# Performance work log

Hardware: AMD Instinct MI355X
Metric: run time of the kernel (lower is better)

Reference implementation:

```python
import jax, jax.numpy as jnp
import numpy as np

D_MODEL = 512
NHEAD = 8
WINDOW = 32  # attends to [i-32, i+32]


def setup_inputs() -> dict:
    key = jax.random.key(0)
    ks = jax.random.split(key, 5)
    B, S, D = 2, 2048, D_MODEL
    return {
        "x": jax.random.normal(ks[0], (B, S, D), dtype=jnp.float32),
        "w_qkv": jax.random.normal(ks[1], (D, 3 * D), dtype=jnp.float32) * 0.02,
        "b_qkv": jax.random.normal(ks[2], (3 * D,), dtype=jnp.float32) * 0.02,
        "w_out": jax.random.normal(ks[3], (D, D), dtype=jnp.float32) * 0.02,
        "b_out": jax.random.normal(ks[4], (D,), dtype=jnp.float32) * 0.02,
    }


def reference(x, w_qkv, b_qkv, w_out, b_out):
    B, S, D = x.shape
    H = NHEAD
    hd = D // H
    w = WINDOW
    W = 2 * w + 1

    qkv = (x @ w_qkv + b_qkv).reshape(B, S, 3, H, hd)
    q, k, v = qkv[:, :, 0], qkv[:, :, 1], qkv[:, :, 2]  # [B,S,H,hd]

    # window indices per query position: [S, W]
    idx = jnp.arange(S)[:, None] + jnp.arange(-w, w + 1)[None, :]
    valid = (idx >= 0) & (idx < S)
    idx_c = jnp.clip(idx, 0, S - 1)

    k_win = k[:, idx_c]  # [B,S,W,H,hd]
    v_win = v[:, idx_c]  # [B,S,W,H,hd]

    scale = 1.0 / (hd ** 0.5)
    scores = jnp.einsum('bshd,bswhd->bshw', q, k_win) * scale  # [B,S,H,W]
    scores = jnp.where(valid[None, :, None, :], scores, -1e9)
    attn = jax.nn.softmax(scores, axis=-1)
    out = jnp.einsum('bshw,bswhd->bshd', attn, v_win).reshape(B, S, D)
    return out @ w_out + b_out
```

## Files before the change

### kernel.cpp

```cpp
#include <hip/hip_runtime.h>


typedef __bf16 bf16x8 __attribute__((ext_vector_type(8)));
typedef float  f32x4  __attribute__((ext_vector_type(4)));
typedef unsigned short u16;
typedef unsigned int   u32;

__device__ __forceinline__ u16 f2bf(float f) {
  u32 u = __builtin_bit_cast(u32, f);
  u += 0x7FFFu + ((u >> 16) & 1u);
  return (u16)(u >> 16);
}
__device__ __forceinline__ float bf2f(u16 u) {
  return __builtin_bit_cast(float, ((u32)u) << 16);
}
__device__ __forceinline__ u32 pack2(u16 a, u16 b) {
  return (u32)a | ((u32)b << 16);
}
__device__ __forceinline__ void glds16(const void* g, void* l) {
  __builtin_amdgcn_global_load_lds(
      (const __attribute__((address_space(1))) void*)g,
      (__attribute__((address_space(3))) void*)l, 16, 0, 0);
}
__device__ __forceinline__ f32x4 mfma16(bf16x8 a, bf16x8 b, f32x4 c) {
  return __builtin_amdgcn_mfma_f32_16x16x32_bf16(a, b, c, 0, 0, 0);
}

__global__ __launch_bounds__(256) void prep_all(
    const float4* __restrict__ X, uint2* __restrict__ XH, uint2* __restrict__ XL,
    const float* __restrict__ Wq, u16* __restrict__ Wqt,
    const float* __restrict__ Wo, u16* __restrict__ Wot) {
  __shared__ float T[32][33];
  const int blk = blockIdx.x, t = threadIdx.x;
  if (blk < 2048) {
    int i = blk * 256 + t;
    float4 v = X[i];
    u16 h0 = f2bf(v.x), h1 = f2bf(v.y), h2 = f2bf(v.z), h3 = f2bf(v.w);
    XH[i] = make_uint2(pack2(h0, h1), pack2(h2, h3));
    XL[i] = make_uint2(pack2(f2bf(v.x - bf2f(h0)), f2bf(v.y - bf2f(h1))),
                       pack2(f2bf(v.z - bf2f(h2)), f2bf(v.w - bf2f(h3))));
    return;
  }
  const float* W;
  u16* Wt;
  int n0, k0, N;
  if (blk < 2816) {
    int idx = blk - 2048;
    W = Wq; Wt = Wqt; N = 1536;
    n0 = (idx % 48) * 32; k0 = (idx / 48) * 32;
  } else {
    int idx = blk - 2816;
    W = Wo; Wt = Wot; N = 512;
    n0 = (idx % 16) * 32; k0 = (idx / 16) * 32;
  }
  const int r = t >> 3, c = (t & 7) * 4;
  float4 v = *(const float4*)&W[(size_t)(k0 + r) * N + n0 + c];
  T[c][r] = v.x; T[c + 1][r] = v.y; T[c + 2][r] = v.z; T[c + 3][r] = v.w;
  __syncthreads();
  u16 a = f2bf(T[r][c]),      b = f2bf(T[r][c + 1]);
  u16 cc = f2bf(T[r][c + 2]), d = f2bf(T[r][c + 3]);
  *(uint2*)&Wt[(size_t)(n0 + r) * 512 + k0 + c] =
      make_uint2(pack2(a, b), pack2(cc, d));
}

__global__ __launch_bounds__(256) void gemm_qkv(
    const u16* __restrict__ Ah, const u16* __restrict__ Al,
    const u16* __restrict__ Bt, const float* __restrict__ bias,
    u16* __restrict__ Qb, u16* __restrict__ Kb, u16* __restrict__ Vb) {
  __shared__ __align__(16) u16 sAh[128 * 32];
  __shared__ __align__(16) u16 sAl[128 * 32];
  __shared__ __align__(16) u16 sB[128 * 32];

  const int t = threadIdx.x, l = t & 63, w = t >> 6;
  const int wm = w >> 1, wn = w & 1;
  const int mBase = blockIdx.y * 128, nBase = blockIdx.x * 128;

  const int q = l >> 2;
  const int kq = ((l & 3) ^ ((q >> 1) & 3)) * 8;
  const int rw0 = w * 32 + q, rw1 = rw0 + 16;
  const u16* gAh0 = Ah + (size_t)(mBase + rw0) * 512 + kq;
  const u16* gAh1 = Ah + (size_t)(mBase + rw1) * 512 + kq;
  const u16* gAl0 = Al + (size_t)(mBase + rw0) * 512 + kq;
  const u16* gAl1 = Al + (size_t)(mBase + rw1) * 512 + kq;
  const u16* gB0  = Bt + (size_t)(nBase + rw0) * 512 + kq;
  const u16* gB1  = Bt + (size_t)(nBase + rw1) * 512 + kq;
  u16* lAh0 = sAh + (w * 32) * 32;
  u16* lAh1 = sAh + (w * 32 + 16) * 32;
  u16* lAl0 = sAl + (w * 32) * 32;
  u16* lAl1 = sAl + (w * 32 + 16) * 32;
  u16* lB0  = sB + (w * 32) * 32;
  u16* lB1  = sB + (w * 32 + 16) * 32;

  const int r15 = l & 15, kg = l >> 4;
  const int pq = (kg ^ ((r15 >> 1) & 3)) * 8;
  int aoff[4], boff[4];
#pragma unroll
  for (int mt = 0; mt < 4; ++mt) aoff[mt] = (wm * 64 + mt * 16 + r15) * 32 + pq;
#pragma unroll
  for (int nt = 0; nt < 4; ++nt) boff[nt] = (wn * 64 + nt * 16 + r15) * 32 + pq;

  f32x4 acc[4][4];
#pragma unroll
  for (int i = 0; i < 4; ++i)
#pragma unroll
    for (int j = 0; j < 4; ++j) acc[i][j] = (f32x4){0.f, 0.f, 0.f, 0.f};

  for (int k0 = 0; k0 < 512; k0 += 32) {
    glds16(gAh0 + k0, lAh0);
    glds16(gAh1 + k0, lAh1);
    glds16(gAl0 + k0, lAl0);
    glds16(gAl1 + k0, lAl1);
    glds16(gB0 + k0, lB0);
    glds16(gB1 + k0, lB1);
    __syncthreads();
    bf16x8 b[4];
#pragma unroll
    for (int nt = 0; nt < 4; ++nt) b[nt] = *(const bf16x8*)(sB + boff[nt]);
#pragma unroll
    for (int mt = 0; mt < 4; ++mt) {
      bf16x8 ah = *(const bf16x8*)(sAh + aoff[mt]);
      bf16x8 al = *(const bf16x8*)(sAl + aoff[mt]);
#pragma unroll
      for (int nt = 0; nt < 4; ++nt) {
        acc[mt][nt] = mfma16(ah, b[nt], acc[mt][nt]);
        acc[mt][nt] = mfma16(al, b[nt], acc[mt][nt]);
      }
    }
    __syncthreads();
  }

  const int lq = l >> 4;
  const int seg = nBase >> 9, colb = nBase & 511;
#pragma unroll
  for (int mt = 0; mt < 4; ++mt) {
    int row0 = mBase + wm * 64 + mt * 16 + lq * 4;
#pragma unroll
    for (int nt = 0; nt < 4; ++nt) {
      int col = wn * 64 + nt * 16 + r15;
      float bv = bias[nBase + col];
      int cc = colb + col;
      if (seg == 0) {
#pragma unroll
        for (int r = 0; r < 4; ++r)
          Qb[(size_t)(row0 + r) * 512 + cc] = f2bf((acc[mt][nt][r] + bv) * 0.125f);
      } else if (seg == 1) {
#pragma unroll
        for (int r = 0; r < 4; ++r)
          Kb[(size_t)(row0 + r) * 512 + cc] = f2bf(acc[mt][nt][r] + bv);
      } else {
#pragma unroll
        for (int r = 0; r < 4; ++r)
          Vb[(size_t)(row0 + r) * 512 + cc] = f2bf(acc[mt][nt][r] + bv);
      }
    }
  }
}

__global__ __launch_bounds__(256) void attn_mfma(
    const u16* __restrict__ Qb, const u16* __restrict__ Kb,
    const u16* __restrict__ Vb, u16* __restrict__ Oh, u16* __restrict__ Ol) {
  const int tile = blockIdx.x, h = blockIdx.y, b = blockIdx.z;
  const int base = tile * 64;
  const size_t hb = (size_t)b * 2048;

  __shared__ __align__(16) u16 Qs[64][72];
  __shared__ __align__(16) u16 Ks[128][72];
  __shared__ __align__(16) u16 Vt[64][136];
  __shared__ __align__(16) u16 Pp[64][136];

  const int t = threadIdx.x, l = t & 63, w = t >> 6;
  const int r15 = l & 15, kg = l >> 4;

  {
    int r = t >> 2, c0 = (t & 3) * 16;
    const uint4* src = (const uint4*)&Qb[(hb + base + r) * 512 + h * 64 + c0];
    *(uint4*)&Qs[r][c0] = src[0];
    *(uint4*)&Qs[r][c0 + 8] = src[1];
  }
  {
    int j = t >> 1, half = (t & 1) * 32;
    int ja = min(max(base - 32 + j, 0), 2047);
    const uint4* src = (const uint4*)&Kb[(hb + ja) * 512 + h * 64 + half];
    uint4* dst = (uint4*)&Ks[j][half];
    dst[0] = src[0]; dst[1] = src[1]; dst[2] = src[2]; dst[3] = src[3];
  }
  {
    int j = t >> 1, ds = (t & 1) * 32;
    int ja = min(max(base - 32 + j, 0), 2047);
    const u16* src = &Vb[(hb + ja) * 512 + h * 64 + ds];
    u16 tmp[32];
    *(uint4*)&tmp[0]  = *(const uint4*)(src);
    *(uint4*)&tmp[8]  = *(const uint4*)(src + 8);
    *(uint4*)&tmp[16] = *(const uint4*)(src + 16);
    *(uint4*)&tmp[24] = *(const uint4*)(src + 24);
#pragma unroll
    for (int i = 0; i < 32; ++i) Vt[ds + i][j] = tmp[i];
  }
  __syncthreads();

  bf16x8 aQ0 = *(const bf16x8*)&Qs[w * 16 + r15][kg * 8];
  bf16x8 aQ1 = *(const bf16x8*)&Qs[w * 16 + r15][32 + kg * 8];
  f32x4 zero = (f32x4){0.f, 0.f, 0.f, 0.f};
  f32x4 sacc[8];
#pragma unroll
  for (int nt = 0; nt < 8; ++nt) {
    bf16x8 b0 = *(const bf16x8*)&Ks[nt * 16 + r15][kg * 8];
    bf16x8 b1 = *(const bf16x8*)&Ks[nt * 16 + r15][32 + kg * 8];
    sacc[nt] = mfma16(aQ0, b0, zero);
    sacc[nt] = mfma16(aQ1, b1, sacc[nt]);
  }

#pragma unroll
  for (int r = 0; r < 4; ++r) {
    int s_abs = base + w * 16 + kg * 4 + r;
    float m = -3.0e38f;
#pragma unroll
    for (int nt = 0; nt < 8; ++nt) {
      int j_abs = base - 32 + nt * 16 + r15;
      int dlt = j_abs - s_abs;
      bool valid = (dlt >= -32) && (dlt <= 32) && (j_abs >= 0) && (j_abs < 2048);
      float v = valid ? sacc[nt][r] : -1.0e9f;
      sacc[nt][r] = v;
      m = fmaxf(m, v);
    }
#pragma unroll
    for (int msk = 1; msk < 16; msk <<= 1) m = fmaxf(m, __shfl_xor(m, msk, 64));
    float s_ = 0.f;
#pragma unroll
    for (int nt = 0; nt < 8; ++nt) {
      float e = __expf(sacc[nt][r] - m);
      sacc[nt][r] = e;
      s_ += e;
    }
#pragma unroll
    for (int msk = 1; msk < 16; msk <<= 1) s_ += __shfl_xor(s_, msk, 64);
    float inv = 1.0f / s_;
#pragma unroll
    for (int nt = 0; nt < 8; ++nt)
      Pp[w * 16 + kg * 4 + r][nt * 16 + r15] = f2bf(sacc[nt][r] * inv);
  }
  __syncthreads();

  bf16x8 aP[4];
#pragma unroll
  for (int kt = 0; kt < 4; ++kt)
    aP[kt] = *(const bf16x8*)&Pp[w * 16 + r15][kt * 32 + kg * 8];
  f32x4 oacc[4];
#pragma unroll
  for (int nt = 0; nt < 4; ++nt) oacc[nt] = zero;
#pragma unroll
  for (int nt = 0; nt < 4; ++nt) {
#pragma unroll
    for (int kt = 0; kt < 4; ++kt) {
      bf16x8 bV = *(const bf16x8*)&Vt[nt * 16 + r15][kt * 32 + kg * 8];
      oacc[nt] = mfma16(aP[kt], bV, oacc[nt]);
    }
  }

#pragma unroll
  for (int nt = 0; nt < 4; ++nt) {
#pragma unroll
    for (int r = 0; r < 4; ++r) {
      float v = oacc[nt][r];
      size_t idx =
          (hb + base + w * 16 + kg * 4 + r) * 512 + h * 64 + nt * 16 + r15;
      u16 hh = f2bf(v);
      Oh[idx] = hh;
      Ol[idx] = f2bf(v - bf2f(hh));
    }
  }
}

__global__ __launch_bounds__(256) void gemm_out(
    const u16* __restrict__ Ah, const u16* __restrict__ Al,
    const u16* __restrict__ Bt, const float* __restrict__ bias,
    float* __restrict__ Cf) {
  __shared__ __align__(16) u16 sAh[64 * 32];
  __shared__ __align__(16) u16 sAl[64 * 32];
  __shared__ __align__(16) u16 sB[128 * 32];

  const int t = threadIdx.x, l = t & 63, w = t >> 6;
  const int wm = w >> 1, wn = w & 1;
  const int mBase = blockIdx.y * 64, nBase = blockIdx.x * 128;

  const int q = l >> 2;
  const int kq = ((l & 3) ^ ((q >> 1) & 3)) * 8;
  const int rA = w * 16 + q;
  const u16* gAh = Ah + (size_t)(mBase + rA) * 512 + kq;
  const u16* gAl = Al + (size_t)(mBase + rA) * 512 + kq;
  const u16* gB0 = Bt + (size_t)(nBase + rA) * 512 + kq;
  const u16* gB1 = Bt + (size_t)(nBase + 64 + rA) * 512 + kq;
  u16* lAh = sAh + w * 512;
  u16* lAl = sAl + w * 512;
  u16* lB0 = sB + w * 512;
  u16* lB1 = sB + (w + 4) * 512;

  const int r15 = l & 15, kg = l >> 4;
  const int pq = (kg ^ ((r15 >> 1) & 3)) * 8;
  const int aoff0 = (wm * 32 + r15) * 32 + pq;
  const int aoff1 = aoff0 + 16 * 32;
  int boff[4];
#pragma unroll
  for (int nt = 0; nt < 4; ++nt) boff[nt] = (wn * 64 + nt * 16 + r15) * 32 + pq;

  f32x4 acc[2][4];
#pragma unroll
  for (int i = 0; i < 2; ++i)
#pragma unroll
    for (int j = 0; j < 4; ++j) acc[i][j] = (f32x4){0.f, 0.f, 0.f, 0.f};

  for (int k0 = 0; k0 < 512; k0 += 32) {
    glds16(gAh + k0, lAh);
    glds16(gAl + k0, lAl);
    glds16(gB0 + k0, lB0);
    glds16(gB1 + k0, lB1);
    __syncthreads();
    bf16x8 a0 = *(const bf16x8*)(sAh + aoff0);
    bf16x8 a1 = *(const bf16x8*)(sAh + aoff1);
    bf16x8 e0 = *(const bf16x8*)(sAl + aoff0);
    bf16x8 e1 = *(const bf16x8*)(sAl + aoff1);
#pragma unroll
    for (int nt = 0; nt < 4; ++nt) {
      bf16x8 bb = *(const bf16x8*)(sB + boff[nt]);
      acc[0][nt] = mfma16(a0, bb, acc[0][nt]);
      acc[0][nt] = mfma16(e0, bb, acc[0][nt]);
      acc[1][nt] = mfma16(a1, bb, acc[1][nt]);
      acc[1][nt] = mfma16(e1, bb, acc[1][nt]);
    }
    __syncthreads();
  }

  const int lq = l >> 4;
#pragma unroll
  for (int mt = 0; mt < 2; ++mt) {
    int row0 = mBase + wm * 32 + mt * 16 + lq * 4;
#pragma unroll
    for (int nt = 0; nt < 4; ++nt) {
      int col = nBase + wn * 64 + nt * 16 + r15;
      float bv = bias[col];
#pragma unroll
      for (int r = 0; r < 4; ++r)
        Cf[(size_t)(row0 + r) * 512 + col] = acc[mt][nt][r] + bv;
    }
  }
}

extern "C" void kernel_launch(void* const* d_in, const int* in_sizes, int n_in,
                              void* d_out, int out_size, void* d_ws, size_t ws_size,
                              hipStream_t stream) {
  const float* x     = (const float*)d_in[0];
  const float* w_qkv = (const float*)d_in[1];
  const float* b_qkv = (const float*)d_in[2];
  const float* w_out = (const float*)d_in[3];
  const float* b_out = (const float*)d_in[4];
  float* out = (float*)d_out;

  char* ws = (char*)d_ws;
  u16* xh  = (u16*)(ws + 0);
  u16* xl  = (u16*)(ws + 4194304);
  u16* wqt = (u16*)(ws + 8388608);
  u16* wot = (u16*)(ws + 9961472);
  u16* qb  = (u16*)(ws + 10485760);
  u16* kb  = (u16*)(ws + 14680064);
  u16* vb  = (u16*)(ws + 18874368);
  u16* aoh = (u16*)(ws + 23068672);
  u16* aol = (u16*)(ws + 27262976);

  prep_all<<<3072, 256, 0, stream>>>((const float4*)x, (uint2*)xh, (uint2*)xl,
                                     w_qkv, wqt, w_out, wot);
  gemm_qkv<<<dim3(12, 32), 256, 0, stream>>>(xh, xl, wqt, b_qkv, qb, kb, vb);
  attn_mfma<<<dim3(32, 8, 2), 256, 0, stream>>>(qb, kb, vb, aoh, aol);
  gemm_out<<<dim3(4, 64), 256, 0, stream>>>(aoh, aol, wot, b_out, out);
}
```

Before: 117.3 us.

## Replace LDS-staged GEMMs with direct global-to-register loads and register prefetch

```diff
diff --git a/kernel.cpp b/kernel.cpp
--- a/kernel.cpp
+++ b/kernel.cpp
@@ -16,11 +16,6 @@
 }
 __device__ __forceinline__ u32 pack2(u16 a, u16 b) {
   return (u32)a | ((u32)b << 16);
-}
-__device__ __forceinline__ void glds16(const void* g, void* l) {
-  __builtin_amdgcn_global_load_lds(
-      (const __attribute__((address_space(1))) void*)g,
-      (__attribute__((address_space(3))) void*)l, 16, 0, 0);
 }
 __device__ __forceinline__ f32x4 mfma16(bf16x8 a, bf16x8 b, f32x4 c) {
   return __builtin_amdgcn_mfma_f32_16x16x32_bf16(a, b, c, 0, 0, 0);
@@ -63,41 +58,27 @@
       make_uint2(pack2(a, b), pack2(cc, d));
 }
 
-__global__ __launch_bounds__(256) void gemm_qkv(
+__global__ __launch_bounds__(256) void gemm_qkv_d(
     const u16* __restrict__ Ah, const u16* __restrict__ Al,
     const u16* __restrict__ Bt, const float* __restrict__ bias,
     u16* __restrict__ Qb, u16* __restrict__ Kb, u16* __restrict__ Vb) {
-  __shared__ __align__(16) u16 sAh[128 * 32];
-  __shared__ __align__(16) u16 sAl[128 * 32];
-  __shared__ __align__(16) u16 sB[128 * 32];
-
   const int t = threadIdx.x, l = t & 63, w = t >> 6;
-  const int wm = w >> 1, wn = w & 1;
-  const int mBase = blockIdx.y * 128, nBase = blockIdx.x * 128;
-
-  const int q = l >> 2;
-  const int kq = ((l & 3) ^ ((q >> 1) & 3)) * 8;
-  const int rw0 = w * 32 + q, rw1 = rw0 + 16;
-  const u16* gAh0 = Ah + (size_t)(mBase + rw0) * 512 + kq;
-  const u16* gAh1 = Ah + (size_t)(mBase + rw1) * 512 + kq;
-  const u16* gAl0 = Al + (size_t)(mBase + rw0) * 512 + kq;
-  const u16* gAl1 = Al + (size_t)(mBase + rw1) * 512 + kq;
-  const u16* gB0  = Bt + (size_t)(nBase + rw0) * 512 + kq;
-  const u16* gB1  = Bt + (size_t)(nBase + rw1) * 512 + kq;
-  u16* lAh0 = sAh + (w * 32) * 32;
-  u16* lAh1 = sAh + (w * 32 + 16) * 32;
-  u16* lAl0 = sAl + (w * 32) * 32;
-  u16* lAl1 = sAl + (w * 32 + 16) * 32;
-  u16* lB0  = sB + (w * 32) * 32;
-  u16* lB1  = sB + (w * 32 + 16) * 32;
-
   const int r15 = l & 15, kg = l >> 4;
-  const int pq = (kg ^ ((r15 >> 1) & 3)) * 8;
-  int aoff[4], boff[4];
-#pragma unroll
-  for (int mt = 0; mt < 4; ++mt) aoff[mt] = (wm * 64 + mt * 16 + r15) * 32 + pq;
-#pragma unroll
-  for (int nt = 0; nt < 4; ++nt) boff[nt] = (wn * 64 + nt * 16 + r15) * 32 + pq;
+  const int mRow0 = blockIdx.y * 256 + w * 64;
+  const int nCol0 = blockIdx.x * 64;
+
+  const u16* pA[4];
+  const u16* pE[4];
+  const u16* pB[4];
+#pragma unroll
+  for (int mt = 0; mt < 4; ++mt) {
+    size_t off = (size_t)(mRow0 + mt * 16 + r15) * 512 + kg * 8;
+    pA[mt] = Ah + off;
+    pE[mt] = Al + off;
+  }
+#pragma unroll
+  for (int nt = 0; nt < 4; ++nt)
+    pB[nt] = Bt + (size_t)(nCol0 + nt * 16 + r15) * 512 + kg * 8;
 
   f32x4 acc[4][4];
 #pragma unroll
@@ -105,40 +86,46 @@
 #pragma unroll
     for (int j = 0; j < 4; ++j) acc[i][j] = (f32x4){0.f, 0.f, 0.f, 0.f};
 
-  for (int k0 = 0; k0 < 512; k0 += 32) {
-    glds16(gAh0 + k0, lAh0);
-    glds16(gAh1 + k0, lAh1);
-    glds16(gAl0 + k0, lAl0);
-    glds16(gAl1 + k0, lAl1);
-    glds16(gB0 + k0, lB0);
-    glds16(gB1 + k0, lB1);
-    __syncthreads();
-    bf16x8 b[4];
-#pragma unroll
-    for (int nt = 0; nt < 4; ++nt) b[nt] = *(const bf16x8*)(sB + boff[nt]);
-#pragma unroll
-    for (int mt = 0; mt < 4; ++mt) {
-      bf16x8 ah = *(const bf16x8*)(sAh + aoff[mt]);
-      bf16x8 al = *(const bf16x8*)(sAl + aoff[mt]);
+  bf16x8 ca[4], ce[4], cb[4];
+#pragma unroll
+  for (int i = 0; i < 4; ++i) {
+    ca[i] = *(const bf16x8*)(pA[i]);
+    ce[i] = *(const bf16x8*)(pE[i]);
+    cb[i] = *(const bf16x8*)(pB[i]);
+  }
+  for (int s = 1; s <= 16; ++s) {
+    bf16x8 na[4], ne[4], nb[4];
+    if (s < 16) {
+      int k0 = s * 32;
+#pragma unroll
+      for (int i = 0; i < 4; ++i) {
+        na[i] = *(const bf16x8*)(pA[i] + k0);
+        ne[i] = *(const bf16x8*)(pE[i] + k0);
+        nb[i] = *(const bf16x8*)(pB[i] + k0);
+      }
+    }
+#pragma unroll
+    for (int mt = 0; mt < 4; ++mt)
 #pragma unroll
       for (int nt = 0; nt < 4; ++nt) {
-        acc[mt][nt] = mfma16(ah, b[nt], acc[mt][nt]);
-        acc[mt][nt] = mfma16(al, b[nt], acc[mt][nt]);
-      }
-    }
-    __syncthreads();
-  }
-
+        acc[mt][nt] = mfma16(ca[mt], cb[nt], acc[mt][nt]);
+        acc[mt][nt] = mfma16(ce[mt], cb[nt], acc[mt][nt]);
+      }
+    if (s < 16) {
+#pragma unroll
+      for (int i = 0; i < 4; ++i) { ca[i] = na[i]; ce[i] = ne[i]; cb[i] = nb[i]; }
+    }
+  }
+
+  const int seg = nCol0 >> 9, cc0 = nCol0 & 511;
   const int lq = l >> 4;
-  const int seg = nBase >> 9, colb = nBase & 511;
 #pragma unroll
   for (int mt = 0; mt < 4; ++mt) {
-    int row0 = mBase + wm * 64 + mt * 16 + lq * 4;
+    int row0 = mRow0 + mt * 16 + lq * 4;
 #pragma unroll
     for (int nt = 0; nt < 4; ++nt) {
-      int col = wn * 64 + nt * 16 + r15;
-      float bv = bias[nBase + col];
-      int cc = colb + col;
+      int cc = cc0 + nt * 16 + r15;
+      float bv = bias[nCol0 + nt * 16 + r15];
       if (seg == 0) {
 #pragma unroll
         for (int r = 0; r < 4; ++r)
@@ -152,6 +139,80 @@
         for (int r = 0; r < 4; ++r)
           Vb[(size_t)(row0 + r) * 512 + cc] = f2bf(acc[mt][nt][r] + bv);
       }
+    }
+  }
+}
+
+__global__ __launch_bounds__(256) void gemm_out_d(
+    const u16* __restrict__ Ah, const u16* __restrict__ Al,
+    const u16* __restrict__ Bt, const float* __restrict__ bias,
+    float* __restrict__ Cf) {
+  const int t = threadIdx.x, l = t & 63, w = t >> 6;
+  const int r15 = l & 15, kg = l >> 4;
+  const int mRow0 = blockIdx.y * 256 + w * 64;
+  const int nCol0 = blockIdx.x * 64;
+
+  const u16* pA[4];
+  const u16* pE[4];
+  const u16* pB[4];
+#pragma unroll
+  for (int mt = 0; mt < 4; ++mt) {
+    size_t off = (size_t)(mRow0 + mt * 16 + r15) * 512 + kg * 8;
+    pA[mt] = Ah + off;
+    pE[mt] = Al + off;
+  }
+#pragma unroll
+  for (int nt = 0; nt < 4; ++nt)
+    pB[nt] = Bt + (size_t)(nCol0 + nt * 16 + r15) * 512 + kg * 8;
+
+  f32x4 acc[4][4];
+#pragma unroll
+  for (int i = 0; i < 4; ++i)
+#pragma unroll
+    for (int j = 0; j < 4; ++j) acc[i][j] = (f32x4){0.f, 0.f, 0.f, 0.f};
+
+  bf16x8 ca[4], ce[4], cb[4];
+#pragma unroll
+  for (int i = 0; i < 4; ++i) {
+    ca[i] = *(const bf16x8*)(pA[i]);
+    ce[i] = *(const bf16x8*)(pE[i]);
+    cb[i] = *(const bf16x8*)(pB[i]);
+  }
+  for (int s = 1; s <= 16; ++s) {
+    bf16x8 na[4], ne[4], nb[4];
+    if (s < 16) {
+      int k0 = s * 32;
+#pragma unroll
+      for (int i = 0; i < 4; ++i) {
+        na[i] = *(const bf16x8*)(pA[i] + k0);
+        ne[i] = *(const bf16x8*)(pE[i] + k0);
+        nb[i] = *(const bf16x8*)(pB[i] + k0);
+      }
+    }
+#pragma unroll
+    for (int mt = 0; mt < 4; ++mt)
+#pragma unroll
+      for (int nt = 0; nt < 4; ++nt) {
+        acc[mt][nt] = mfma16(ca[mt], cb[nt], acc[mt][nt]);
+        acc[mt][nt] = mfma16(ce[mt], cb[nt], acc[mt][nt]);
+      }
+    if (s < 16) {
+#pragma unroll
+      for (int i = 0; i < 4; ++i) { ca[i] = na[i]; ce[i] = ne[i]; cb[i] = nb[i]; }
+    }
+  }
+
+  const int lq = l >> 4;
+#pragma unroll
+  for (int mt = 0; mt < 4; ++mt) {
+    int row0 = mRow0 + mt * 16 + lq * 4;
+#pragma unroll
+    for (int nt = 0; nt < 4; ++nt) {
+      int col = nCol0 + nt * 16 + r15;
+      float bv = bias[col];
+#pragma unroll
+      for (int r = 0; r < 4; ++r)
+        Cf[(size_t)(row0 + r) * 512 + col] = acc[mt][nt][r] + bv;
     }
   }
 }
@@ -267,80 +328,6 @@
       u16 hh = f2bf(v);
       Oh[idx] = hh;
       Ol[idx] = f2bf(v - bf2f(hh));
-    }
-  }
-}
-
-__global__ __launch_bounds__(256) void gemm_out(
-    const u16* __restrict__ Ah, const u16* __restrict__ Al,
-    const u16* __restrict__ Bt, const float* __restrict__ bias,
-    float* __restrict__ Cf) {
-  __shared__ __align__(16) u16 sAh[64 * 32];
-  __shared__ __align__(16) u16 sAl[64 * 32];
-  __shared__ __align__(16) u16 sB[128 * 32];
-
-  const int t = threadIdx.x, l = t & 63, w = t >> 6;
-  const int wm = w >> 1, wn = w & 1;
-  const int mBase = blockIdx.y * 64, nBase = blockIdx.x * 128;
-
-  const int q = l >> 2;
-  const int kq = ((l & 3) ^ ((q >> 1) & 3)) * 8;
-  const int rA = w * 16 + q;
-  const u16* gAh = Ah + (size_t)(mBase + rA) * 512 + kq;
-  const u16* gAl = Al + (size_t)(mBase + rA) * 512 + kq;
-  const u16* gB0 = Bt + (size_t)(nBase + rA) * 512 + kq;
-  const u16* gB1 = Bt + (size_t)(nBase + 64 + rA) * 512 + kq;
-  u16* lAh = sAh + w * 512;
-  u16* lAl = sAl + w * 512;
-  u16* lB0 = sB + w * 512;
-  u16* lB1 = sB + (w + 4) * 512;
-
-  const int r15 = l & 15, kg = l >> 4;
-  const int pq = (kg ^ ((r15 >> 1) & 3)) * 8;
-  const int aoff0 = (wm * 32 + r15) * 32 + pq;
-  const int aoff1 = aoff0 + 16 * 32;
-  int boff[4];
-#pragma unroll
-  for (int nt = 0; nt < 4; ++nt) boff[nt] = (wn * 64 + nt * 16 + r15) * 32 + pq;
-
-  f32x4 acc[2][4];
-#pragma unroll
-  for (int i = 0; i < 2; ++i)
-#pragma unroll
-    for (int j = 0; j < 4; ++j) acc[i][j] = (f32x4){0.f, 0.f, 0.f, 0.f};
-
-  for (int k0 = 0; k0 < 512; k0 += 32) {
-    glds16(gAh + k0, lAh);
-    glds16(gAl + k0, lAl);
-    glds16(gB0 + k0, lB0);
-    glds16(gB1 + k0, lB1);
-    __syncthreads();
-    bf16x8 a0 = *(const bf16x8*)(sAh + aoff0);
-    bf16x8 a1 = *(const bf16x8*)(sAh + aoff1);
-    bf16x8 e0 = *(const bf16x8*)(sAl + aoff0);
-    bf16x8 e1 = *(const bf16x8*)(sAl + aoff1);
-#pragma unroll
-    for (int nt = 0; nt < 4; ++nt) {
-      bf16x8 bb = *(const bf16x8*)(sB + boff[nt]);
-      acc[0][nt] = mfma16(a0, bb, acc[0][nt]);
-      acc[0][nt] = mfma16(e0, bb, acc[0][nt]);
-      acc[1][nt] = mfma16(a1, bb, acc[1][nt]);
-      acc[1][nt] = mfma16(e1, bb, acc[1][nt]);
-    }
-    __syncthreads();
-  }
-
-  const int lq = l >> 4;
-#pragma unroll
-  for (int mt = 0; mt < 2; ++mt) {
-    int row0 = mBase + wm * 32 + mt * 16 + lq * 4;
-#pragma unroll
-    for (int nt = 0; nt < 4; ++nt) {
-      int col = nBase + wn * 64 + nt * 16 + r15;
-      float bv = bias[col];
-#pragma unroll
-      for (int r = 0; r < 4; ++r)
-        Cf[(size_t)(row0 + r) * 512 + col] = acc[mt][nt][r] + bv;
     }
   }
 }
@@ -368,7 +355,7 @@
 
   prep_all<<<3072, 256, 0, stream>>>((const float4*)x, (uint2*)xh, (uint2*)xl,
                                      w_qkv, wqt, w_out, wot);
-  gemm_qkv<<<dim3(12, 32), 256, 0, stream>>>(xh, xl, wqt, b_qkv, qb, kb, vb);
+  gemm_qkv_d<<<dim3(24, 16), 256, 0, stream>>>(xh, xl, wqt, b_qkv, qb, kb, vb);
   attn_mfma<<<dim3(32, 8, 2), 256, 0, stream>>>(qb, kb, vb, aoh, aol);
-  gemm_out<<<dim3(4, 64), 256, 0, stream>>>(aoh, aol, wot, b_out, out);
-}
+  gemm_out_d<<<dim3(8, 16), 256, 0, stream>>>(aoh, aol, wot, b_out, out);
+}
```

New measurement: 153.1 us. 30.5% more time.
